# Kernel tuning notes

Hardware: AMD Instinct MI355X
Metric: run time of the kernel (lower is better)

The kernel has to match this reference:

```python
import jax, jax.numpy as jnp
import numpy as np

B, C, H, W = 4, 256, 64, 64
CQK = C // 8  # 32


def setup_inputs() -> dict:
    key = jax.random.key(0)
    ks = jax.random.split(key, 8)
    s = 0.05
    return {
        "x": jax.random.normal(ks[0], (B, C, H, W), dtype=jnp.float32),
        "wq": jax.random.normal(ks[1], (CQK, C), dtype=jnp.float32) * s,
        "bq": jax.random.normal(ks[2], (CQK,), dtype=jnp.float32) * s,
        "wk": jax.random.normal(ks[3], (CQK, C), dtype=jnp.float32) * s,
        "bk": jax.random.normal(ks[4], (CQK,), dtype=jnp.float32) * s,
        "wv": jax.random.normal(ks[5], (C, C), dtype=jnp.float32) * s,
        "bv": jax.random.normal(ks[6], (C,), dtype=jnp.float32) * s,
        "gamma": jax.random.normal(ks[7], (1,), dtype=jnp.float32),
    }


def reference(x, wq, bq, wk, bk, wv, bv, gamma):
    b, c, h, w = x.shape
    n = h * w
    xf = x.reshape(b, c, n)  # (B, C, N)
    # 1x1 conv + bias + ReLU (Conv2d wrapper default activate='relu')
    q = jax.nn.relu(jnp.einsum('oc,bcn->bon', wq, xf) + bq[:, None])  # (B, CQK, N)
    k = jax.nn.relu(jnp.einsum('oc,bcn->bon', wk, xf) + bk[:, None])  # (B, CQK, N)
    v = jax.nn.relu(jnp.einsum('oc,bcn->bon', wv, xf) + bv[:, None])  # (B, C, N)
    # energy[b, i, j] = sum_c q[b, c, i] * k[b, c, j]
    energy = jnp.einsum('bci,bcj->bij', q, k)  # (B, N, N)
    attention = jax.nn.softmax(energy, axis=-1)
    # out[b, c, i] = sum_j v[b, c, j] * attention[b, i, j]
    out = jnp.einsum('bcj,bij->bci', v, attention)  # (B, C, N)
    out = out.reshape(b, c, h, w)
    return gamma[0] * out + x
```

## Files before the change

kernel.cpp:

```cpp
#include <hip/hip_runtime.h>
#include <stdint.h>


#define NB 4
#define CD 256
#define ND 4096
#define CQ 32
#define LOG2E 1.4426950408889634f

typedef __attribute__((ext_vector_type(4))) float f32x4;
typedef __attribute__((ext_vector_type(8))) _Float16 f16x8;
typedef __attribute__((ext_vector_type(4))) unsigned short u16x4;
typedef __attribute__((ext_vector_type(2))) unsigned int u32x2;
typedef __attribute__((ext_vector_type(4))) int i32x4;

static __device__ __forceinline__ unsigned short f2h(float f) {
    union { _Float16 h; unsigned short u; } cv; cv.h = (_Float16)f; return cv.u;
}
static __device__ __forceinline__ float fexp2(float xv) {
    float r; asm("v_exp_f32 %0, %1" : "=v"(r) : "v"(xv)); return r;
}

__global__ __launch_bounds__(256) void wcvt_kernel(
    const float* __restrict__ wq, const float* __restrict__ wk,
    const float* __restrict__ wv, unsigned short* __restrict__ Wh)
{
    const int idx = blockIdx.x * 256 + threadIdx.x;
    const int m = idx >> 6, kq = (idx & 63) << 2;
    const float* src = (m < 32) ? (wq + (size_t)m * CD + kq)
                     : (m < 64) ? (wk + (size_t)(m - 32) * CD + kq)
                                : (wv + (size_t)(m - 64) * CD + kq);
    const f32x4 v = *reinterpret_cast<const f32x4*>(src);
    u16x4 h;
#pragma unroll
    for (int u = 0; u < 4; ++u) h[u] = f2h(v[u]);
    *reinterpret_cast<u16x4*>(Wh + (size_t)m * CD + kq) = h;
}

__global__ __launch_bounds__(640) void proj_kernel(
    const float* __restrict__ x, const unsigned short* __restrict__ Wh,
    const float* __restrict__ bq, const float* __restrict__ bk,
    const float* __restrict__ bv,
    unsigned short* __restrict__ Qt, unsigned short* __restrict__ Kt,
    unsigned short* __restrict__ Vp)
{
    __shared__ __align__(16) unsigned char xls[64 * 512];

    const int tid = threadIdx.x;
    const int lane = tid & 63;
    const int w = __builtin_amdgcn_readfirstlane(tid >> 6);
    const int m16 = lane & 15, g4 = lane >> 4;
    const int b = blockIdx.x >> 6, n0 = (blockIdx.x & 63) << 6;

    {
        const float* xb = x + (size_t)b * CD * ND + n0;
#pragma unroll 1
        for (int idx = tid; idx < 4096; idx += 640) {
            const int c = idx >> 4, nq = (idx & 15) << 2;
            const f32x4 v = *reinterpret_cast<const f32x4*>(xb + (size_t)c * ND + nq);
#pragma unroll
            for (int r = 0; r < 4; ++r) {
                const int row = nq + r;
                const int ad = (row * 512 + c * 2) ^ ((row & 7) << 4);
                *reinterpret_cast<unsigned short*>(&xls[ad]) = f2h(v[r]);
            }
        }
    }
    __syncthreads();

    f32x4 acc[2][4];
#pragma unroll
    for (int a = 0; a < 2; ++a)
#pragma unroll
        for (int c = 0; c < 4; ++c) acc[a][c] = (f32x4){0.f, 0.f, 0.f, 0.f};

    const unsigned short* Wrow = Wh + (size_t)(w * 32 + m16) * CD;
    const int bswz = (m16 & 7) << 4;
    const bool qk = (w < 2);

#pragma unroll
    for (int ks = 0; ks < 8; ++ks) {
        const int ko = ks * 32 + g4 * 8;
        f16x8 af[2], bf[4];
#pragma unroll
        for (int ms = 0; ms < 2; ++ms)
            af[ms] = *reinterpret_cast<const f16x8*>(Wrow + (size_t)ms * 16 * CD + ko);
#pragma unroll
        for (int ns = 0; ns < 4; ++ns) {
            const int ad = ((ns * 16 + m16) * 512 + ko * 2) ^ bswz;
            bf[ns] = *reinterpret_cast<const f16x8*>(&xls[ad]);
        }
        if (qk) {
#pragma unroll
            for (int ms = 0; ms < 2; ++ms)
#pragma unroll
                for (int ns = 0; ns < 4; ++ns)
                    acc[ms][ns] = __builtin_amdgcn_mfma_f32_16x16x32_f16(
                        af[ms], bf[ns], acc[ms][ns], 0, 0, 0);
        } else {
#pragma unroll
            for (int ms = 0; ms < 2; ++ms)
#pragma unroll
                for (int ns = 0; ns < 4; ++ns)
                    acc[ms][ns] = __builtin_amdgcn_mfma_f32_16x16x32_f16(
                        bf[ns], af[ms], acc[ms][ns], 0, 0, 0);
        }
    }

    if (w == 0) {
#pragma unroll
        for (int ms = 0; ms < 2; ++ms) {
            const int mb = ms * 16 + g4 * 4;
            const f32x4 bias = *reinterpret_cast<const f32x4*>(bq + mb);
#pragma unroll
            for (int ns = 0; ns < 4; ++ns) {
                const int n = n0 + ns * 16 + m16;
                u16x4 h;
#pragma unroll
                for (int r = 0; r < 4; ++r)
                    h[r] = f2h(fmaxf(acc[ms][ns][r] + bias[r], 0.f) * LOG2E);
                *reinterpret_cast<u16x4*>(Qt + ((size_t)(b * ND + n)) * CQ + mb) = h;
            }
        }
    } else if (w == 1) {
#pragma unroll
        for (int ms = 0; ms < 2; ++ms) {
            const int mb = ms * 16 + g4 * 4;
            const f32x4 bias = *reinterpret_cast<const f32x4*>(bk + mb);
#pragma unroll
            for (int ns = 0; ns < 4; ++ns) {
                const int n = n0 + ns * 16 + m16;
                u16x4 h;
#pragma unroll
                for (int r = 0; r < 4; ++r)
                    h[r] = f2h(fmaxf(acc[ms][ns][r] + bias[r], 0.f));
                *reinterpret_cast<u16x4*>(Kt + ((size_t)(b * ND + n)) * CQ + mb) = h;
            }
        }
    } else {
        const int cbase = (w - 2) * 32;
#pragma unroll
        for (int ms = 0; ms < 2; ++ms) {
            const int c = cbase + ms * 16 + m16;
            const float bval = bv[c];
#pragma unroll
            for (int ns = 0; ns < 4; ++ns) {
                const int n = n0 + ns * 16 + g4 * 4;
                u16x4 h;
#pragma unroll
                for (int r = 0; r < 4; ++r)
                    h[r] = f2h(fmaxf(acc[ms][ns][r] + bval, 0.f));
                unsigned short* dst = Vp
                    + ((size_t)((b * 128 + (n >> 5)) * 16 + (c >> 4))) * 512
                    + ((((n >> 3) & 3) * 16 + (c & 15)) * 8) + (n & 7);
                *reinterpret_cast<u16x4*>(dst) = h;
            }
        }
    }
}

__global__ __launch_bounds__(768) void attn_kernel(
    const unsigned short* __restrict__ Qt, const unsigned short* __restrict__ Kt,
    const unsigned short* __restrict__ Vp, const float* __restrict__ x,
    const float* __restrict__ gamma, float* __restrict__ out)
{
    __shared__ __align__(16) unsigned char smem[68864];
    __shared__ int gctr[3];
    float* scales = reinterpret_cast<float*>(smem + 49152);
    int*   flags  = reinterpret_cast<int*>(smem + 50688);
    float* Ocomb  = reinterpret_cast<float*>(smem);
    float* mfin   = reinterpret_cast<float*>(smem + 66560);
    float* lfin   = reinterpret_cast<float*>(smem + 67328);
    float* wfac   = reinterpret_cast<float*>(smem + 68096);

    const int tid  = threadIdx.x;
    const int lane = tid & 63;
    const int w12  = __builtin_amdgcn_readfirstlane(tid >> 6);
    const int g    = (w12 >= 8) ? 2 : (w12 >> 2);
    const int ws   = (w12 >= 8) ? (w12 - 8) : (w12 & 3);
    const int m16  = lane & 15;
    const int g4   = lane >> 4;
    const int wg   = (blockIdx.x & 7) * 32 + (blockIdx.x >> 3);
    const int b    = wg >> 6;
    const int i0   = (wg & 63) << 6;

    if (tid < 3) gctr[tid] = 0;
    __syncthreads();

    const f16x8 qfrag = *reinterpret_cast<const f16x8*>(
        Qt + ((size_t)(b * ND + i0 + ws * 16 + m16)) * CQ + g4 * 8);
    const unsigned short* kb = Kt + ((size_t)(b * ND + m16)) * CQ + g4 * 8;
    const unsigned short* vpc =
        Vp + ((size_t)(b * 128 * 16 + ws * 4)) * 512 + lane * 8;

    f32x4 oacc[4][4];
#pragma unroll
    for (int a = 0; a < 4; ++a)
#pragma unroll
        for (int c = 0; c < 4; ++c) oacc[a][c] = (f32x4){0.f, 0.f, 0.f, 0.f};
    float mrow = -1e30f;
    float lrow = 0.f;
    const f32x4 zero4 = {0.f, 0.f, 0.f, 0.f};

    const int cbase  = (g == 0) ? 0 : (g == 1) ? 22 : 43;
    const int nsteps = (g == 0) ? 22 : 21;
    const int irow   = ws * 16 + m16;
    const int iswz   = (m16 & 7) << 4;

    auto LOADK = [&](f16x8 (&kr)[4], int j) {
#pragma unroll
        for (int t = 0; t < 4; ++t)
            kr[t] = *reinterpret_cast<const f16x8*>(kb + (size_t)(j + t * 16) * CQ);
    };

    auto GSYNC = [&](int s) {
        asm volatile("s_waitcnt lgkmcnt(0)" ::: "memory");
        if (lane == 0) atomicAdd(&gctr[g], 1);
        const int tgt = (s + 1) * 4;
        int cv = __builtin_amdgcn_readfirstlane(*(volatile int*)&gctr[g]);
        while (cv < tgt) {
            __builtin_amdgcn_s_sleep(1);
            cv = __builtin_amdgcn_readfirstlane(*(volatile int*)&gctr[g]);
        }
    };

    auto STEP = [&](int s, f16x8 (&kc)[4], f16x8 (&kn)[4]) {
        const int j0  = (cbase + s) * 64;
        const int par = s & 1;
        unsigned char* pb = smem + g * 16384 + par * 8192;

        const int jblk0 = j0 >> 5;
        f16x8 vf[2][4];
#pragma unroll
        for (int jhh = 0; jhh < 2; ++jhh)
#pragma unroll
            for (int cs = 0; cs < 4; ++cs)
                vf[jhh][cs] = *reinterpret_cast<const f16x8*>(
                    vpc + (size_t)((jblk0 + jhh) * 16 + cs) * 512);
        const int jn = (s + 1 < nsteps) ? (j0 + 64) : cbase * 64;
        LOADK(kn, jn);

        f32x4 sv[4];
#pragma unroll
        for (int t = 0; t < 4; ++t)
            sv[t] = __builtin_amdgcn_mfma_f32_16x16x32_f16(kc[t], qfrag, zero4, 0, 0, 0);

        float pm = sv[0][0];
#pragma unroll
        for (int t = 0; t < 4; ++t)
#pragma unroll
            for (int r = 0; r < 4; ++r) pm = fmaxf(pm, sv[t][r]);
        float sc = 1.0f;
        int myresc = 0;
        if (__ballot(pm <= mrow + 8.0f) != ~0ull) {
            float pr = fmaxf(pm, __shfl_xor(pm, 16));
            pr = fmaxf(pr, __shfl_xor(pr, 32));
            const float mnew = fmaxf(mrow, pr);
            sc = fexp2(mrow - mnew);
            mrow = mnew;
            myresc = 1;
        }
        float rs = 0.f;
#pragma unroll
        for (int t = 0; t < 4; ++t)
#pragma unroll
            for (int r = 0; r < 4; ++r) { sv[t][r] = fexp2(sv[t][r] - mrow); rs += sv[t][r]; }
        lrow = lrow * sc + rs;

#pragma unroll
        for (int t = 0; t < 4; ++t) {
            u32x2 pw;
            pw[0] = __builtin_bit_cast(unsigned int,
                        __builtin_amdgcn_cvt_pkrtz(sv[t][0], sv[t][1]));
            pw[1] = __builtin_bit_cast(unsigned int,
                        __builtin_amdgcn_cvt_pkrtz(sv[t][2], sv[t][3]));
            const int lo = (irow * 128 + t * 32 + g4 * 8) ^ iswz;
            *reinterpret_cast<u32x2*>(pb + lo) = pw;
        }
        if (g4 == 0)   scales[(g * 2 + par) * 64 + irow] = sc;
        if (lane == 0) flags[(g * 2 + par) * 4 + ws] = myresc;

        GSYNC(s);

        const i32x4 fl = *reinterpret_cast<const i32x4*>(flags + (g * 2 + par) * 4);
        const int anyresc = __builtin_amdgcn_readfirstlane(fl[0] | fl[1] | fl[2] | fl[3]);
        if (anyresc) {
#pragma unroll
            for (int is = 0; is < 4; ++is) {
                const f32x4 sr = *reinterpret_cast<const f32x4*>(
                    scales + (g * 2 + par) * 64 + is * 16 + g4 * 4);
#pragma unroll
                for (int r = 0; r < 4; ++r)
#pragma unroll
                    for (int cs = 0; cs < 4; ++cs) oacc[is][cs][r] *= sr[r];
            }
        }

        __builtin_amdgcn_s_setprio(1);
#pragma unroll
        for (int jhh = 0; jhh < 2; ++jhh) {
#pragma unroll
            for (int is = 0; is < 4; ++is) {
                const int lo = ((is * 16 + m16) * 128 + jhh * 64 + g4 * 16) ^ iswz;
                const f16x8 pf = *reinterpret_cast<const f16x8*>(pb + lo);
#pragma unroll
                for (int cs = 0; cs < 4; ++cs)
                    oacc[is][cs] = __builtin_amdgcn_mfma_f32_16x16x32_f16(
                        pf, vf[jhh][cs], oacc[is][cs], 0, 0, 0);
            }
        }
        __builtin_amdgcn_s_setprio(0);
    };

    f16x8 kA[4], kB[4];
    LOADK(kA, cbase * 64);

#pragma unroll 1
    for (int s2 = 0; s2 < 11; ++s2) {
        const int s0 = 2 * s2, s1 = s0 + 1;
        if (s0 >= nsteps) break;
        STEP(s0, kA, kB);
        if (s1 >= nsteps) break;
        STEP(s1, kB, kA);
    }

    lrow += __shfl_xor(lrow, 16);
    lrow += __shfl_xor(lrow, 32);
    if (g4 == 0) { mfin[g * 64 + irow] = mrow; lfin[g * 64 + irow] = lrow; }
    __syncthreads();

    if (tid < 192) {
        const int gg = tid >> 6, i = tid & 63;
        const float m0 = mfin[i], m1 = mfin[64 + i], m2 = mfin[128 + i];
        const float M  = fmaxf(fmaxf(m0, m1), m2);
        const float e0 = fexp2(m0 - M), e1 = fexp2(m1 - M), e2 = fexp2(m2 - M);
        const float den = lfin[i] * e0 + lfin[64 + i] * e1 + lfin[128 + i] * e2;
        wfac[gg * 64 + i] = ((gg == 0) ? e0 : (gg == 1) ? e1 : e2) / den;
    }
    __syncthreads();

#pragma unroll
    for (int gg = 0; gg < 3; ++gg) {
        if (g == gg) {
#pragma unroll
            for (int is = 0; is < 4; ++is) {
                const f32x4 f = *reinterpret_cast<const f32x4*>(
                    wfac + g * 64 + is * 16 + g4 * 4);
#pragma unroll
                for (int cs = 0; cs < 4; ++cs)
#pragma unroll
                    for (int r = 0; r < 4; ++r) {
                        const int i = is * 16 + g4 * 4 + r;
                        const int c = ws * 64 + cs * 16 + m16;
                        if (gg == 0) Ocomb[i * 260 + c]  = oacc[is][cs][r] * f[r];
                        else         Ocomb[i * 260 + c] += oacc[is][cs][r] * f[r];
                    }
            }
        }
        __syncthreads();
    }

    const float gm = gamma[0];
#pragma unroll 1
    for (int q = tid; q < 4096; q += 768) {
        const int c  = q >> 4;
        const int ib = (q & 15) * 4;
        f32x4 o;
#pragma unroll
        for (int u = 0; u < 4; ++u) o[u] = Ocomb[(ib + u) * 260 + c];
        const size_t idx = ((size_t)(b * CD + c)) * ND + i0 + ib;
        const f32x4 xv = *reinterpret_cast<const f32x4*>(x + idx);
        f32x4 res;
#pragma unroll
        for (int u = 0; u < 4; ++u) res[u] = gm * o[u] + xv[u];
        *reinterpret_cast<f32x4*>(out + idx) = res;
    }
}

extern "C" void kernel_launch(void* const* d_in, const int* in_sizes, int n_in,
                              void* d_out, int out_size, void* d_ws, size_t ws_size,
                              hipStream_t stream) {
    const float* x     = (const float*)d_in[0];
    const float* wq    = (const float*)d_in[1];
    const float* bq    = (const float*)d_in[2];
    const float* wk    = (const float*)d_in[3];
    const float* bk    = (const float*)d_in[4];
    const float* wv    = (const float*)d_in[5];
    const float* bv    = (const float*)d_in[6];
    const float* gamma = (const float*)d_in[7];

    unsigned short* Qt = (unsigned short*)d_ws;
    unsigned short* Kt = Qt + (size_t)NB * ND * CQ;
    unsigned short* Vp = Kt + (size_t)NB * ND * CQ;
    unsigned short* Wh = Vp + (size_t)NB * CD * ND;
    float* out = (float*)d_out;

    wcvt_kernel<<<dim3(80),      dim3(256), 0, stream>>>(wq, wk, wv, Wh);
    proj_kernel<<<dim3(NB * 64), dim3(640), 0, stream>>>(x, Wh, bq, bk, bv, Qt, Kt, Vp);
    attn_kernel<<<dim3(NB * 64), dim3(768), 0, stream>>>(Qt, Kt, Vp, x, gamma, out);
}
```

Baseline: 67.36 us.

## Split attention into producer softmax waves and consumer PV waves with ring buffer

Replaces the three-way key-split (each group doing QK, softmax and PV, then combining partial results) with warp specialization. Four producer waves compute scores and softmax for all 64 key tiles into a 4-slot LDS ring. Eight consumer waves each own 32 output channels and run the P·V MFMAs, coordinated by per-wave step counters in shared memory. This removes the cross-group max/sum merge and cuts LDS use, aiming to overlap exp work with matrix work. The output is staged through LDS in fp16 before the residual add, which loses some precision, and the spin-wait handshakes could serialize the producer and consumer waves.

```diff
diff --git a/kernel.cpp b/kernel.cpp
--- a/kernel.cpp
+++ b/kernel.cpp
@@ -11,14 +11,21 @@
 typedef __attribute__((ext_vector_type(4))) float f32x4;
 typedef __attribute__((ext_vector_type(8))) _Float16 f16x8;
 typedef __attribute__((ext_vector_type(4))) unsigned short u16x4;
+typedef __attribute__((ext_vector_type(8))) unsigned short u16x8;
 typedef __attribute__((ext_vector_type(2))) unsigned int u32x2;
 typedef __attribute__((ext_vector_type(4))) int i32x4;
 
 static __device__ __forceinline__ unsigned short f2h(float f) {
     union { _Float16 h; unsigned short u; } cv; cv.h = (_Float16)f; return cv.u;
 }
+static __device__ __forceinline__ float h2f(unsigned short u) {
+    union { unsigned short u; _Float16 h; } cv; cv.u = u; return (float)cv.h;
+}
 static __device__ __forceinline__ float fexp2(float xv) {
     float r; asm("v_exp_f32 %0, %1" : "=v"(r) : "v"(xv)); return r;
+}
+static __device__ __forceinline__ unsigned int pk2(float a, float b) {
+    return __builtin_bit_cast(unsigned int, __builtin_amdgcn_cvt_pkrtz(a, b));
 }
 
 __global__ __launch_bounds__(256) void wcvt_kernel(
@@ -164,216 +171,246 @@
     const unsigned short* __restrict__ Vp, const float* __restrict__ x,
     const float* __restrict__ gamma, float* __restrict__ out)
 {
-    __shared__ __align__(16) unsigned char smem[68864];
-    __shared__ int gctr[3];
-    float* scales = reinterpret_cast<float*>(smem + 49152);
-    int*   flags  = reinterpret_cast<int*>(smem + 50688);
-    float* Ocomb  = reinterpret_cast<float*>(smem);
-    float* mfin   = reinterpret_cast<float*>(smem + 66560);
-    float* lfin   = reinterpret_cast<float*>(smem + 67328);
-    float* wfac   = reinterpret_cast<float*>(smem + 68096);
+    __shared__ __align__(16) unsigned char smem[35072];
+    __shared__ int prodstep[4];
+    __shared__ int consstep[8];
+    float* scales = reinterpret_cast<float*>(smem + 32768);
+    int*   flags  = reinterpret_cast<int*>(smem + 33792);
+    float* lfin   = reinterpret_cast<float*>(smem + 34816);
 
     const int tid  = threadIdx.x;
     const int lane = tid & 63;
     const int w12  = __builtin_amdgcn_readfirstlane(tid >> 6);
-    const int g    = (w12 >= 8) ? 2 : (w12 >> 2);
-    const int ws   = (w12 >= 8) ? (w12 - 8) : (w12 & 3);
     const int m16  = lane & 15;
     const int g4   = lane >> 4;
     const int wg   = (blockIdx.x & 7) * 32 + (blockIdx.x >> 3);
     const int b    = wg >> 6;
     const int i0   = (wg & 63) << 6;
 
-    if (tid < 3) gctr[tid] = 0;
+    if (tid < 4) prodstep[tid] = 0;
+    if (tid < 8) consstep[tid] = 0;
     __syncthreads();
 
-    const f16x8 qfrag = *reinterpret_cast<const f16x8*>(
-        Qt + ((size_t)(b * ND + i0 + ws * 16 + m16)) * CQ + g4 * 8);
-    const unsigned short* kb = Kt + ((size_t)(b * ND + m16)) * CQ + g4 * 8;
-    const unsigned short* vpc =
-        Vp + ((size_t)(b * 128 * 16 + ws * 4)) * 512 + lane * 8;
-
-    f32x4 oacc[4][4];
-#pragma unroll
-    for (int a = 0; a < 4; ++a)
-#pragma unroll
-        for (int c = 0; c < 4; ++c) oacc[a][c] = (f32x4){0.f, 0.f, 0.f, 0.f};
-    float mrow = -1e30f;
-    float lrow = 0.f;
-    const f32x4 zero4 = {0.f, 0.f, 0.f, 0.f};
-
-    const int cbase  = (g == 0) ? 0 : (g == 1) ? 22 : 43;
-    const int nsteps = (g == 0) ? 22 : 21;
-    const int irow   = ws * 16 + m16;
-    const int iswz   = (m16 & 7) << 4;
-
-    auto LOADK = [&](f16x8 (&kr)[4], int j) {
-#pragma unroll
-        for (int t = 0; t < 4; ++t)
-            kr[t] = *reinterpret_cast<const f16x8*>(kb + (size_t)(j + t * 16) * CQ);
-    };
-
-    auto GSYNC = [&](int s) {
-        asm volatile("s_waitcnt lgkmcnt(0)" ::: "memory");
-        if (lane == 0) atomicAdd(&gctr[g], 1);
-        const int tgt = (s + 1) * 4;
-        int cv = __builtin_amdgcn_readfirstlane(*(volatile int*)&gctr[g]);
-        while (cv < tgt) {
-            __builtin_amdgcn_s_sleep(1);
-            cv = __builtin_amdgcn_readfirstlane(*(volatile int*)&gctr[g]);
-        }
-    };
-
-    auto STEP = [&](int s, f16x8 (&kc)[4], f16x8 (&kn)[4]) {
-        const int j0  = (cbase + s) * 64;
-        const int par = s & 1;
-        unsigned char* pb = smem + g * 16384 + par * 8192;
-
-        const int jblk0 = j0 >> 5;
-        f16x8 vf[2][4];
-#pragma unroll
-        for (int jhh = 0; jhh < 2; ++jhh)
-#pragma unroll
-            for (int cs = 0; cs < 4; ++cs)
-                vf[jhh][cs] = *reinterpret_cast<const f16x8*>(
-                    vpc + (size_t)((jblk0 + jhh) * 16 + cs) * 512);
-        const int jn = (s + 1 < nsteps) ? (j0 + 64) : cbase * 64;
-        LOADK(kn, jn);
-
-        f32x4 sv[4];
-#pragma unroll
-        for (int t = 0; t < 4; ++t)
-            sv[t] = __builtin_amdgcn_mfma_f32_16x16x32_f16(kc[t], qfrag, zero4, 0, 0, 0);
-
-        float pm = sv[0][0];
-#pragma unroll
-        for (int t = 0; t < 4; ++t)
-#pragma unroll
-            for (int r = 0; r < 4; ++r) pm = fmaxf(pm, sv[t][r]);
-        float sc = 1.0f;
-        int myresc = 0;
-        if (__ballot(pm <= mrow + 8.0f) != ~0ull) {
-            float pr = fmaxf(pm, __shfl_xor(pm, 16));
-            pr = fmaxf(pr, __shfl_xor(pr, 32));
-            const float mnew = fmaxf(mrow, pr);
-            sc = fexp2(mrow - mnew);
-            mrow = mnew;
-            myresc = 1;
-        }
-        float rs = 0.f;
-#pragma unroll
-        for (int t = 0; t < 4; ++t)
-#pragma unroll
-            for (int r = 0; r < 4; ++r) { sv[t][r] = fexp2(sv[t][r] - mrow); rs += sv[t][r]; }
-        lrow = lrow * sc + rs;
-
-#pragma unroll
-        for (int t = 0; t < 4; ++t) {
-            u32x2 pw;
-            pw[0] = __builtin_bit_cast(unsigned int,
-                        __builtin_amdgcn_cvt_pkrtz(sv[t][0], sv[t][1]));
-            pw[1] = __builtin_bit_cast(unsigned int,
-                        __builtin_amdgcn_cvt_pkrtz(sv[t][2], sv[t][3]));
-            const int lo = (irow * 128 + t * 32 + g4 * 8) ^ iswz;
-            *reinterpret_cast<u32x2*>(pb + lo) = pw;
-        }
-        if (g4 == 0)   scales[(g * 2 + par) * 64 + irow] = sc;
-        if (lane == 0) flags[(g * 2 + par) * 4 + ws] = myresc;
-
-        GSYNC(s);
-
-        const i32x4 fl = *reinterpret_cast<const i32x4*>(flags + (g * 2 + par) * 4);
-        const int anyresc = __builtin_amdgcn_readfirstlane(fl[0] | fl[1] | fl[2] | fl[3]);
-        if (anyresc) {
-#pragma unroll
-            for (int is = 0; is < 4; ++is) {
-                const f32x4 sr = *reinterpret_cast<const f32x4*>(
-                    scales + (g * 2 + par) * 64 + is * 16 + g4 * 4);
-#pragma unroll
-                for (int r = 0; r < 4; ++r)
-#pragma unroll
-                    for (int cs = 0; cs < 4; ++cs) oacc[is][cs][r] *= sr[r];
-            }
-        }
-
-        __builtin_amdgcn_s_setprio(1);
-#pragma unroll
-        for (int jhh = 0; jhh < 2; ++jhh) {
-#pragma unroll
-            for (int is = 0; is < 4; ++is) {
-                const int lo = ((is * 16 + m16) * 128 + jhh * 64 + g4 * 16) ^ iswz;
-                const f16x8 pf = *reinterpret_cast<const f16x8*>(pb + lo);
-#pragma unroll
-                for (int cs = 0; cs < 4; ++cs)
-                    oacc[is][cs] = __builtin_amdgcn_mfma_f32_16x16x32_f16(
-                        pf, vf[jhh][cs], oacc[is][cs], 0, 0, 0);
-            }
-        }
-        __builtin_amdgcn_s_setprio(0);
-    };
-
-    f16x8 kA[4], kB[4];
-    LOADK(kA, cbase * 64);
-
+    if (w12 < 4) {
+        const int ws   = w12;
+        const int irow = ws * 16 + m16;
+        const int iswz = (m16 & 7) << 4;
+
+        const f16x8 qfrag = *reinterpret_cast<const f16x8*>(
+            Qt + ((size_t)(b * ND + i0 + irow)) * CQ + g4 * 8);
+        const unsigned short* kb = Kt + ((size_t)(b * ND + m16)) * CQ + g4 * 8;
+
+        float mrow = -1e30f;
+        float lrow = 0.f;
+        const f32x4 zero4 = {0.f, 0.f, 0.f, 0.f};
+
+        auto LOADK = [&](f16x8 (&kr)[4], int j) {
+#pragma unroll
+            for (int t = 0; t < 4; ++t)
+                kr[t] = *reinterpret_cast<const f16x8*>(kb + (size_t)(j + t * 16) * CQ);
+        };
+
+        auto PSTEP = [&](int k, f16x8 (&kc)[4], f16x8 (&kn)[4]) {
+            const int jn = ((k + 1) & 63) * 64;
+            LOADK(kn, jn);
+
+            f32x4 sv[4];
+#pragma unroll
+            for (int t = 0; t < 4; ++t)
+                sv[t] = __builtin_amdgcn_mfma_f32_16x16x32_f16(kc[t], qfrag, zero4, 0, 0, 0);
+
+            float pm = sv[0][0];
+#pragma unroll
+            for (int t = 0; t < 4; ++t)
+#pragma unroll
+                for (int r = 0; r < 4; ++r) pm = fmaxf(pm, sv[t][r]);
+            float sc = 1.0f;
+            int myresc = 0;
+            if (__ballot(pm <= mrow + 8.0f) != ~0ull) {
+                float pr = fmaxf(pm, __shfl_xor(pm, 16));
+                pr = fmaxf(pr, __shfl_xor(pr, 32));
+                const float mnew = fmaxf(mrow, pr);
+                sc = fexp2(mrow - mnew);
+                mrow = mnew;
+                myresc = 1;
+            }
+            float rs = 0.f;
+#pragma unroll
+            for (int t = 0; t < 4; ++t)
+#pragma unroll
+                for (int r = 0; r < 4; ++r) { sv[t][r] = fexp2(sv[t][r] - mrow); rs += sv[t][r]; }
+            lrow = lrow * sc + rs;
+
+            if (k >= 4) {
+                const int tgt = k - 3;
+                int mn;
+                do {
+                    volatile int* cs = consstep;
+                    int m0 = cs[0], m1 = cs[1], m2 = cs[2], m3 = cs[3];
+                    int m4 = cs[4], m5 = cs[5], m6 = cs[6], m7 = cs[7];
+                    mn = min(min(min(m0, m1), min(m2, m3)),
+                             min(min(m4, m5), min(m6, m7)));
+                    if (mn < tgt) __builtin_amdgcn_s_sleep(1);
+                } while (mn < tgt);
+                asm volatile("" ::: "memory");
+                __builtin_amdgcn_sched_barrier(0);
+            }
+
+            unsigned char* pb = smem + (k & 3) * 8192;
+#pragma unroll
+            for (int t = 0; t < 4; ++t) {
+                u32x2 pw;
+                pw[0] = pk2(sv[t][0], sv[t][1]);
+                pw[1] = pk2(sv[t][2], sv[t][3]);
+                const int lo = (irow * 128 + t * 32 + g4 * 8) ^ iswz;
+                *reinterpret_cast<u32x2*>(pb + lo) = pw;
+            }
+            if (g4 == 0)   scales[(k & 3) * 64 + irow] = sc;
+            if (lane == 0) flags[(k & 3) * 4 + ws] = myresc;
+
+            asm volatile("s_waitcnt lgkmcnt(0)" ::: "memory");
+            if (lane == 0) *(volatile int*)&prodstep[ws] = k + 1;
+        };
+
+        f16x8 kA[4], kB[4];
+        LOADK(kA, 0);
 #pragma unroll 1
-    for (int s2 = 0; s2 < 11; ++s2) {
-        const int s0 = 2 * s2, s1 = s0 + 1;
-        if (s0 >= nsteps) break;
-        STEP(s0, kA, kB);
-        if (s1 >= nsteps) break;
-        STEP(s1, kB, kA);
-    }
-
-    lrow += __shfl_xor(lrow, 16);
-    lrow += __shfl_xor(lrow, 32);
-    if (g4 == 0) { mfin[g * 64 + irow] = mrow; lfin[g * 64 + irow] = lrow; }
-    __syncthreads();
-
-    if (tid < 192) {
-        const int gg = tid >> 6, i = tid & 63;
-        const float m0 = mfin[i], m1 = mfin[64 + i], m2 = mfin[128 + i];
-        const float M  = fmaxf(fmaxf(m0, m1), m2);
-        const float e0 = fexp2(m0 - M), e1 = fexp2(m1 - M), e2 = fexp2(m2 - M);
-        const float den = lfin[i] * e0 + lfin[64 + i] * e1 + lfin[128 + i] * e2;
-        wfac[gg * 64 + i] = ((gg == 0) ? e0 : (gg == 1) ? e1 : e2) / den;
-    }
-    __syncthreads();
-
-#pragma unroll
-    for (int gg = 0; gg < 3; ++gg) {
-        if (g == gg) {
-#pragma unroll
-            for (int is = 0; is < 4; ++is) {
-                const f32x4 f = *reinterpret_cast<const f32x4*>(
-                    wfac + g * 64 + is * 16 + g4 * 4);
-#pragma unroll
-                for (int cs = 0; cs < 4; ++cs)
-#pragma unroll
-                    for (int r = 0; r < 4; ++r) {
-                        const int i = is * 16 + g4 * 4 + r;
-                        const int c = ws * 64 + cs * 16 + m16;
-                        if (gg == 0) Ocomb[i * 260 + c]  = oacc[is][cs][r] * f[r];
-                        else         Ocomb[i * 260 + c] += oacc[is][cs][r] * f[r];
-                    }
-            }
-        }
+        for (int k2 = 0; k2 < 32; ++k2) {
+            PSTEP(2 * k2,     kA, kB);
+            PSTEP(2 * k2 + 1, kB, kA);
+        }
+
+        lrow += __shfl_xor(lrow, 16);
+        lrow += __shfl_xor(lrow, 32);
+        if (g4 == 0) lfin[irow] = lrow;
         __syncthreads();
-    }
-
-    const float gm = gamma[0];
+        __syncthreads();
+
+        const float gm = gamma[0];
+        unsigned short* Oc = reinterpret_cast<unsigned short*>(smem);
 #pragma unroll 1
-    for (int q = tid; q < 4096; q += 768) {
-        const int c  = q >> 4;
-        const int ib = (q & 15) * 4;
-        f32x4 o;
-#pragma unroll
-        for (int u = 0; u < 4; ++u) o[u] = Ocomb[(ib + u) * 260 + c];
-        const size_t idx = ((size_t)(b * CD + c)) * ND + i0 + ib;
-        const f32x4 xv = *reinterpret_cast<const f32x4*>(x + idx);
-        f32x4 res;
-#pragma unroll
-        for (int u = 0; u < 4; ++u) res[u] = gm * o[u] + xv[u];
-        *reinterpret_cast<f32x4*>(out + idx) = res;
+        for (int q = tid; q < 2048; q += 768) {
+            const int c = q >> 3, i8 = (q & 7) * 8;
+            const u16x8 o = *reinterpret_cast<const u16x8*>(&Oc[c * 68 + i8]);
+            const size_t idx = ((size_t)(b * CD + c)) * ND + i0 + i8;
+            const f32x4 xa = *reinterpret_cast<const f32x4*>(x + idx);
+            const f32x4 xb2 = *reinterpret_cast<const f32x4*>(x + idx + 4);
+            f32x4 ra, rb;
+#pragma unroll
+            for (int u = 0; u < 4; ++u) {
+                ra[u] = gm * h2f(o[u]) + xa[u];
+                rb[u] = gm * h2f(o[u + 4]) + xb2[u];
+            }
+            *reinterpret_cast<f32x4*>(out + idx)     = ra;
+            *reinterpret_cast<f32x4*>(out + idx + 4) = rb;
+        }
+    } else {
+        const int cw   = w12 - 4;
+        const int cb   = cw * 32;
+        const int iswz = (m16 & 7) << 4;
+
+        const unsigned short* vpc =
+            Vp + ((size_t)(b * 2048 + cw * 2)) * 512 + lane * 8;
+
+        f32x4 oacc[4][2];
+#pragma unroll
+        for (int a = 0; a < 4; ++a)
+#pragma unroll
+            for (int c = 0; c < 2; ++c) oacc[a][c] = (f32x4){0.f, 0.f, 0.f, 0.f};
+
+#pragma unroll 1
+        for (int k = 0; k < 64; ++k) {
+            f16x8 vf[2][2];
+#pragma unroll
+            for (int jhh = 0; jhh < 2; ++jhh)
+#pragma unroll
+                for (int cs = 0; cs < 2; ++cs)
+                    vf[jhh][cs] = *reinterpret_cast<const f16x8*>(
+                        vpc + (size_t)((2 * k + jhh) * 16 + cs) * 512);
+
+            {
+                const int tgt = k + 1;
+                int mn;
+                do {
+                    volatile int* ps = prodstep;
+                    int m0 = ps[0], m1 = ps[1], m2 = ps[2], m3 = ps[3];
+                    mn = min(min(m0, m1), min(m2, m3));
+                    if (mn < tgt) __builtin_amdgcn_s_sleep(1);
+                } while (mn < tgt);
+                asm volatile("" ::: "memory");
+                __builtin_amdgcn_sched_barrier(0);
+            }
+
+            const int slot = k & 3;
+            const i32x4 fl = *reinterpret_cast<const i32x4*>(flags + slot * 4);
+            const int anyresc = __builtin_amdgcn_readfirstlane(fl[0] | fl[1] | fl[2] | fl[3]);
+            if (anyresc) {
+#pragma unroll
+                for (int is = 0; is < 4; ++is) {
+                    const f32x4 sr = *reinterpret_cast<const f32x4*>(
+                        scales + slot * 64 + is * 16 + g4 * 4);
+#pragma unroll
+                    for (int r = 0; r < 4; ++r)
+#pragma unroll
+                        for (int cs = 0; cs < 2; ++cs) oacc[is][cs][r] *= sr[r];
+                }
+            }
+
+            unsigned char* pb = smem + slot * 8192;
+            __builtin_amdgcn_s_setprio(1);
+#pragma unroll
+            for (int jhh = 0; jhh < 2; ++jhh) {
+#pragma unroll
+                for (int is = 0; is < 4; ++is) {
+                    const int lo = ((is * 16 + m16) * 128 + jhh * 64 + g4 * 16) ^ iswz;
+                    const f16x8 pf = *reinterpret_cast<const f16x8*>(pb + lo);
+#pragma unroll
+                    for (int cs = 0; cs < 2; ++cs)
+                        oacc[is][cs] = __builtin_amdgcn_mfma_f32_16x16x32_f16(
+                            pf, vf[jhh][cs], oacc[is][cs], 0, 0, 0);
+                }
+            }
+            __builtin_amdgcn_s_setprio(0);
+
+            asm volatile("s_waitcnt lgkmcnt(0)" ::: "memory");
+            if (lane == 0) *(volatile int*)&consstep[cw] = k + 1;
+        }
+
+        __syncthreads();
+
+        unsigned short* Oc = reinterpret_cast<unsigned short*>(smem);
+#pragma unroll
+        for (int is = 0; is < 4; ++is) {
+            const f32x4 rv = *reinterpret_cast<const f32x4*>(lfin + is * 16 + g4 * 4);
+            const f32x4 ri = {1.0f / rv[0], 1.0f / rv[1], 1.0f / rv[2], 1.0f / rv[3]};
+#pragma unroll
+            for (int cs = 0; cs < 2; ++cs) {
+                const int c = cb + cs * 16 + m16;
+                u32x2 pw;
+                pw[0] = pk2(oacc[is][cs][0] * ri[0], oacc[is][cs][1] * ri[1]);
+                pw[1] = pk2(oacc[is][cs][2] * ri[2], oacc[is][cs][3] * ri[3]);
+                *reinterpret_cast<u32x2*>(&Oc[c * 68 + is * 16 + g4 * 4]) = pw;
+            }
+        }
+        __syncthreads();
+
+        const float gm = gamma[0];
+#pragma unroll 1
+        for (int q = tid; q < 2048; q += 768) {
+            const int c = q >> 3, i8 = (q & 7) * 8;
+            const u16x8 o = *reinterpret_cast<const u16x8*>(&Oc[c * 68 + i8]);
+            const size_t idx = ((size_t)(b * CD + c)) * ND + i0 + i8;
+            const f32x4 xa = *reinterpret_cast<const f32x4*>(x + idx);
+            const f32x4 xb2 = *reinterpret_cast<const f32x4*>(x + idx + 4);
+            f32x4 ra, rb;
+#pragma unroll
+            for (int u = 0; u < 4; ++u) {
+                ra[u] = gm * h2f(o[u]) + xa[u];
+                rb[u] = gm * h2f(o[u + 4]) + xb2[u];
+            }
+            *reinterpret_cast<f32x4*>(out + idx)     = ra;
+            *reinterpret_cast<f32x4*>(out + idx + 4) = rb;
+        }
     }
 }
 
```

New measurement: 78.53 us. 1.17x slower.

## Software-pipeline QK softmax one step ahead of PV accumulation across wave sync

Applied to the files above, without the earlier changes.

Restructures the attention loop so that each step computes the QK scores and softmax for the next key block before waiting on the group counter. The packed probabilities are stored to LDS and the counter is signalled after the PV MFMAs, splitting the old combined barrier into a separate arrive and wait. The aim is to overlap the exp/softmax work and the barrier latency with the PV matrix work. In exchange it raises register pressure, since packed probabilities, scale and flag are carried between steps, and K loads are now issued two blocks ahead.

```diff
diff --git a/kernel.cpp b/kernel.cpp
--- a/kernel.cpp
+++ b/kernel.cpp
@@ -19,6 +19,9 @@
 }
 static __device__ __forceinline__ float fexp2(float xv) {
     float r; asm("v_exp_f32 %0, %1" : "=v"(r) : "v"(xv)); return r;
+}
+static __device__ __forceinline__ unsigned int pk2(float a, float b) {
+    return __builtin_bit_cast(unsigned int, __builtin_amdgcn_cvt_pkrtz(a, b));
 }
 
 __global__ __launch_bounds__(256) void wcvt_kernel(
@@ -213,38 +216,15 @@
             kr[t] = *reinterpret_cast<const f16x8*>(kb + (size_t)(j + t * 16) * CQ);
     };
 
-    auto GSYNC = [&](int s) {
-        asm volatile("s_waitcnt lgkmcnt(0)" ::: "memory");
-        if (lane == 0) atomicAdd(&gctr[g], 1);
-        const int tgt = (s + 1) * 4;
-        int cv = __builtin_amdgcn_readfirstlane(*(volatile int*)&gctr[g]);
-        while (cv < tgt) {
-            __builtin_amdgcn_s_sleep(1);
-            cv = __builtin_amdgcn_readfirstlane(*(volatile int*)&gctr[g]);
-        }
-    };
-
-    auto STEP = [&](int s, f16x8 (&kc)[4], f16x8 (&kn)[4]) {
-        const int j0  = (cbase + s) * 64;
-        const int par = s & 1;
-        unsigned char* pb = smem + g * 16384 + par * 8192;
-
-        const int jblk0 = j0 >> 5;
-        f16x8 vf[2][4];
-#pragma unroll
-        for (int jhh = 0; jhh < 2; ++jhh)
-#pragma unroll
-            for (int cs = 0; cs < 4; ++cs)
-                vf[jhh][cs] = *reinterpret_cast<const f16x8*>(
-                    vpc + (size_t)((jblk0 + jhh) * 16 + cs) * 512);
-        const int jn = (s + 1 < nsteps) ? (j0 + 64) : cbase * 64;
-        LOADK(kn, jn);
-
+    u32x2 pwn[4];
+    float scn   = 1.0f;
+    int   rescn = 0;
+
+    auto QKSM = [&](f16x8 (&kc)[4]) {
         f32x4 sv[4];
 #pragma unroll
         for (int t = 0; t < 4; ++t)
             sv[t] = __builtin_amdgcn_mfma_f32_16x16x32_f16(kc[t], qfrag, zero4, 0, 0, 0);
-
         float pm = sv[0][0];
 #pragma unroll
         for (int t = 0; t < 4; ++t)
@@ -262,26 +242,63 @@
         }
         float rs = 0.f;
 #pragma unroll
-        for (int t = 0; t < 4; ++t)
+        for (int t = 0; t < 4; ++t) {
 #pragma unroll
             for (int r = 0; r < 4; ++r) { sv[t][r] = fexp2(sv[t][r] - mrow); rs += sv[t][r]; }
+            pwn[t][0] = pk2(sv[t][0], sv[t][1]);
+            pwn[t][1] = pk2(sv[t][2], sv[t][3]);
+        }
         lrow = lrow * sc + rs;
-
+        scn = sc;
+        rescn = myresc;
+    };
+
+    auto PSTORE = [&](int s) {
+        const int par = s & 1;
+        unsigned char* pb = smem + g * 16384 + par * 8192;
 #pragma unroll
         for (int t = 0; t < 4; ++t) {
-            u32x2 pw;
-            pw[0] = __builtin_bit_cast(unsigned int,
-                        __builtin_amdgcn_cvt_pkrtz(sv[t][0], sv[t][1]));
-            pw[1] = __builtin_bit_cast(unsigned int,
-                        __builtin_amdgcn_cvt_pkrtz(sv[t][2], sv[t][3]));
             const int lo = (irow * 128 + t * 32 + g4 * 8) ^ iswz;
-            *reinterpret_cast<u32x2*>(pb + lo) = pw;
-        }
-        if (g4 == 0)   scales[(g * 2 + par) * 64 + irow] = sc;
-        if (lane == 0) flags[(g * 2 + par) * 4 + ws] = myresc;
-
-        GSYNC(s);
-
+            *reinterpret_cast<u32x2*>(pb + lo) = pwn[t];
+        }
+        if (g4 == 0)   scales[(g * 2 + par) * 64 + irow] = scn;
+        if (lane == 0) flags[(g * 2 + par) * 4 + ws] = rescn;
+        asm volatile("s_waitcnt lgkmcnt(0)" ::: "memory");
+        if (lane == 0) atomicAdd(&gctr[g], 1);
+    };
+
+    auto WAITC = [&](int s) {
+        const int tgt = (s + 1) * 4;
+        int cv = __builtin_amdgcn_readfirstlane(*(volatile int*)&gctr[g]);
+        while (cv < tgt) {
+            __builtin_amdgcn_s_sleep(1);
+            cv = __builtin_amdgcn_readfirstlane(*(volatile int*)&gctr[g]);
+        }
+        asm volatile("" ::: "memory");
+    };
+
+    auto STEP = [&](int s, f16x8 (&kc)[4], f16x8 (&kn)[4]) {
+        const int j0 = (cbase + s) * 64;
+        const int jblk0 = j0 >> 5;
+        f16x8 vf[2][4];
+#pragma unroll
+        for (int jhh = 0; jhh < 2; ++jhh)
+#pragma unroll
+            for (int cs = 0; cs < 4; ++cs)
+                vf[jhh][cs] = *reinterpret_cast<const f16x8*>(
+                    vpc + (size_t)((jblk0 + jhh) * 16 + cs) * 512);
+
+        const bool have_next = (s + 1 < nsteps);
+        if (have_next) {
+            const int jn2 = (s + 2 < nsteps) ? (j0 + 128) : cbase * 64;
+            LOADK(kn, jn2);
+            QKSM(kc);
+        }
+
+        WAITC(s);
+
+        const int par = s & 1;
+        unsigned char* pb = smem + g * 16384 + par * 8192;
         const i32x4 fl = *reinterpret_cast<const i32x4*>(flags + (g * 2 + par) * 4);
         const int anyresc = __builtin_amdgcn_readfirstlane(fl[0] | fl[1] | fl[2] | fl[3]);
         if (anyresc) {
@@ -310,10 +327,15 @@
             }
         }
         __builtin_amdgcn_s_setprio(0);
+
+        if (have_next) PSTORE(s + 1);
     };
 
     f16x8 kA[4], kB[4];
     LOADK(kA, cbase * 64);
+    QKSM(kA);
+    PSTORE(0);
+    LOADK(kA, (nsteps > 1) ? (cbase * 64 + 64) : cbase * 64);
 
 #pragma unroll 1
     for (int s2 = 0; s2 < 11; ++s2) {
```

Result: slower. 76.13 us (+13.0%).
